# Optimization experiments

Hardware: AMD Instinct MI355X
Metric: run time of the kernel (lower is better)

The kernel has to match this reference:

```python
import jax, jax.numpy as jnp
import numpy as np

EPS = 1e-5
K = 20  # knn3(K=20) is hardcoded in the torch module


def _bn_lrelu(x, g, b, axes):
    # training-mode BatchNorm (batch statistics) + LeakyReLU(0.2)
    m = jnp.mean(x, axis=axes, keepdims=True)
    v = jnp.var(x, axis=axes, keepdims=True)
    y = (x - m) * jax.lax.rsqrt(v + EPS) * g + b
    return jax.nn.leaky_relu(y, 0.2)


def _pool(pts, feat, num_pool):
    # pts: [B,N,3] coords, feat: [B,N,C]. KNN of first num_pool points vs all
    # points, gather neighbor features, max over the K neighbors.
    sub = pts[:, :num_pool]                                   # [B,M,3]
    d2 = (jnp.sum(sub * sub, -1)[:, :, None]
          + jnp.sum(pts * pts, -1)[:, None, :]
          - 2.0 * jnp.einsum('bmd,bnd->bmn', sub, pts))       # [B,M,N]
    idx = jax.lax.top_k(-d2, K)[1]                            # [B,M,K]
    gathered = jax.vmap(lambda f, i: f[i])(feat, idx)         # [B,M,K,C]
    return sub, jnp.max(gathered, axis=2)                     # [B,M,C]


def setup_inputs() -> dict:
    key = jax.random.key(0)
    ks = jax.random.split(key, 16)
    f32 = jnp.float32
    def n(k, shape, s):
        return jax.random.normal(k, shape, dtype=f32) * s
    emb = 1024
    return {
        'x': jax.random.normal(ks[0], (16, 3, 4096), dtype=f32),
        'w1': n(ks[1], (64, 3), 0.5), 'g1': jnp.ones(64, f32), 'b1': jnp.zeros(64, f32),
        'w2': n(ks[2], (64, 64), 0.12), 'g2': jnp.ones(64, f32), 'b2': jnp.zeros(64, f32),
        'w3': n(ks[3], (128, 64), 0.12), 'g3': jnp.ones(128, f32), 'b3': jnp.zeros(128, f32),
        'w4': n(ks[4], (256, 128), 0.09), 'g4': jnp.ones(256, f32), 'b4': jnp.zeros(256, f32),
        'w5': n(ks[5], (emb, 512), 0.045), 'g5': jnp.ones(emb, f32), 'b5': jnp.zeros(emb, f32),
        'l1w': n(ks[6], (512, 2 * emb), 0.022), 'g6': jnp.ones(512, f32), 'b6': jnp.zeros(512, f32),
        'l2w': n(ks[7], (256, 512), 0.045), 'l2b': jnp.zeros(256, f32),
        'g7': jnp.ones(256, f32), 'b7': jnp.zeros(256, f32),
        'l3w': n(ks[8], (40, 256), 0.06), 'l3b': jnp.zeros(40, f32),
    }


def reference(x, w1, g1, b1, w2, g2, b2, w3, g3, b3, w4, g4, b4,
              w5, g5, b5, l1w, g6, b6, l2w, l2b, g7, b7, l3w, l3b):
    B, _, N = x.shape
    pts = jnp.transpose(x, (0, 2, 1))                 # [B,N,3]
    f = _bn_lrelu(pts @ w1.T, g1, b1, (0, 1))         # conv1 -> [B,N,64]
    p, f = _pool(pts, f, N // 4)
    _, x1 = _pool(p, f, N // 64)                      # [B,N/64,64]
    f = _bn_lrelu(f @ w2.T, g2, b2, (0, 1))           # conv2
    p, f = _pool(p, f, N // 16)
    _, x2 = _pool(p, f, N // 64)                      # [B,N/64,64]
    f = _bn_lrelu(f @ w3.T, g3, b3, (0, 1))           # conv3
    p, f = _pool(p, f, N // 32)
    _, x3 = _pool(p, f, N // 64)                      # [B,N/64,128]
    f = _bn_lrelu(f @ w4.T, g4, b4, (0, 1))           # conv4
    p, f = _pool(p, f, N // 64)                       # [B,N/64,256]
    h = jnp.concatenate([x1, x2, x3, f], axis=-1)     # [B,N/64,512]
    h = _bn_lrelu(h @ w5.T, g5, b5, (0, 1))           # conv5 -> [B,N/64,emb]
    h = jnp.concatenate([jnp.max(h, axis=1), jnp.mean(h, axis=1)], axis=-1)
    h = _bn_lrelu(h @ l1w.T, g6, b6, (0,))            # linear1 (no bias)
    h = _bn_lrelu(h @ l2w.T + l2b, g7, b7, (0,))      # linear2; dropout = eval identity
    return h @ l3w.T + l3b                            # [B,40]
```

## Files before the change

kernel.cpp:

```cpp
#include <hip/hip_runtime.h>

#define BN_EPS 1e-5f
#define KNN 20

static inline int ceildiv(int a, int b) { return (a + b - 1) / b; }

__device__ __forceinline__ unsigned long long shflxor64(unsigned long long v, int m, int w) {
    int lo = __shfl_xor((int)(unsigned)(v & 0xffffffffull), m, w);
    int hi = __shfl_xor((int)(unsigned)(v >> 32), m, w);
    return ((unsigned long long)(unsigned)hi << 32) | (unsigned)lo;
}

__global__ void moments3_kernel(const float* __restrict__ x, int N,
                                float* __restrict__ part ,
                                float4* __restrict__ pk ) {
    int b = blockIdx.x;
    int chunk = blockIdx.y;
    int t = threadIdx.x;
    int n0 = chunk * (N >> 2);
    int n1 = n0 + (N >> 2);
    const float* xb = x + (size_t)b * 3 * N;
    float m[9] = {0, 0, 0, 0, 0, 0, 0, 0, 0};
    for (int n = n0 + t; n < n1; n += 256) {
        float px = xb[n], py = xb[N + n], pz = xb[2 * N + n];
        float nr = px * px + py * py + pz * pz;
        pk[(size_t)b * N + n] = make_float4(px, py, pz, nr);
        m[0] += px; m[1] += py; m[2] += pz;
        m[3] += px * px; m[4] += py * py; m[5] += pz * pz;
        m[6] += px * py; m[7] += px * pz; m[8] += py * pz;
    }
#pragma unroll
    for (int o = 32; o; o >>= 1)
#pragma unroll
        for (int i = 0; i < 9; ++i) m[i] += __shfl_down(m[i], o);
    __shared__ float red[4][9];
    if ((t & 63) == 0)
#pragma unroll
        for (int i = 0; i < 9; ++i) red[t >> 6][i] = m[i];
    __syncthreads();
    if (t == 0) {
#pragma unroll
        for (int i = 0; i < 9; ++i)
            part[(b * 4 + chunk) * 9 + i] = red[0][i] + red[1][i] + red[2][i] + red[3][i];
    }
}

__global__ void knn_all_kernel(const float4* __restrict__ pk, int Nstride,
                               int* __restrict__ iA, int* __restrict__ iB,
                               int* __restrict__ iC, int* __restrict__ iD,
                               int* __restrict__ iE, int* __restrict__ iF) {
    int b = blockIdx.y;
    int bx = blockIdx.x;
    int M, N; int* out; int qbase;
    if (bx < 128)      { M = 1024; N = 4096; out = iA; qbase = bx * 8; }
    else if (bx < 136) { M = 64;   N = 1024; out = iB; qbase = (bx - 128) * 8; }
    else if (bx < 168) { M = 256;  N = 1024; out = iC; qbase = (bx - 136) * 8; }
    else if (bx < 176) { M = 64;   N = 256;  out = iD; qbase = (bx - 168) * 8; }
    else if (bx < 192) { M = 128;  N = 256;  out = iE; qbase = (bx - 176) * 8; }
    else               { M = 64;   N = 128;  out = iF; qbase = (bx - 192) * 8; }
    int wave = threadIdx.x >> 6;
    int lane = threadIdx.x & 63;
    int sl = lane & 31;
    int half = lane >> 5;
    int q = qbase + wave * 2 + half;
    const float4* pb = pk + (size_t)b * Nstride;
    float4 qp = pb[q];

    auto dist = [&](int j) -> float {
        float4 c = pb[j];
        return qp.w + c.w - 2.f * (qp.x * c.x + qp.y * c.y + qp.z * c.z);
    };

    int up_addr = ((sl == 0) ? lane : (lane - 1)) << 2;
    int wd_addr = (19 + (half << 5)) << 2;
    int segbyte = half << 7;

    unsigned long long lk;
    {
        float d2 = dist(sl);
        unsigned u = __float_as_uint(d2);
        unsigned ok = (u & 0x80000000u) ? ~u : (u | 0x80000000u);
        lk = ((unsigned long long)ok << 32) | (unsigned)sl;
    }
#pragma unroll
    for (int size = 2; size <= 32; size <<= 1) {
#pragma unroll
        for (int stride = size >> 1; stride >= 1; stride >>= 1) {
            unsigned long long p = shflxor64(lk, stride, 32);
            bool ascend = (sl & size) == 0;
            bool low = (sl & stride) == 0;
            bool keepMin = (ascend == low);
            bool pLess = p < lk;
            lk = (keepMin == pLess) ? p : lk;
        }
    }
    unsigned okey = (unsigned)(lk >> 32);
    unsigned du = (okey & 0x80000000u) ? (okey ^ 0x80000000u) : ~okey;
    float ld = __uint_as_float(du);
    int li = (int)(unsigned)(lk & 0xffffffffull);
    float wd = __uint_as_float(__builtin_amdgcn_ds_bpermute(wd_addr, (int)__float_as_uint(ld)));

    auto insert2 = [&](float dc, int jb, unsigned long long msk) {
        unsigned mlo = (unsigned)msk, mhi = (unsigned)(msk >> 32);
        while (mlo | mhi) {
            int slo = __ffs((int)mlo) - 1;
            int shi = __ffs((int)mhi) - 1;
            int srcl = half ? shi : slo;
            int addr = ((srcl & 31) << 2) + segbyte;
            float d = __uint_as_float(__builtin_amdgcn_ds_bpermute(addr, (int)__float_as_uint(dc)));
            if (srcl < 0) d = 3.4e38f;
            int id = jb + (srcl & 31);
            float up_d = __uint_as_float(__builtin_amdgcn_ds_bpermute(up_addr, (int)__float_as_uint(ld)));
            int up_i = __builtin_amdgcn_ds_bpermute(up_addr, li);
            bool c = d < ld;
            bool cp = (sl != 0) && (d < up_d);
            ld = c ? (cp ? up_d : d) : ld;
            li = c ? (cp ? up_i : id) : li;
            mlo &= mlo - 1;
            mhi &= mhi - 1;
        }
    };

    {
        float dc = dist(32 + sl);
        unsigned long long m = __ballot(dc < wd);
        if (m) {
            insert2(dc, 32, m);
            wd = __uint_as_float(__builtin_amdgcn_ds_bpermute(wd_addr, (int)__float_as_uint(ld)));
        }
    }
    for (int j0 = 64; j0 < N; j0 += 64) {
        float dc0 = dist(j0 + sl);
        float dc1 = dist(j0 + 32 + sl);
        unsigned long long m0 = __ballot(dc0 < wd);
        unsigned long long m1 = __ballot(dc1 < wd);
        if (m0 | m1) {
            if (m0) insert2(dc0, j0, m0);
            if (m1) insert2(dc1, j0 + 32, m1);
            wd = __uint_as_float(__builtin_amdgcn_ds_bpermute(wd_addr, (int)__float_as_uint(ld)));
        }
    }
    if (sl < KNN) out[((size_t)b * M + q) * KNN + sl] = li;
}

__global__ void pool1_kernel(const float4* __restrict__ pk, int N, const int* __restrict__ idxA,
                             const float* __restrict__ w1, const float* __restrict__ mom,
                             const float* __restrict__ g, const float* __restrict__ bb,
                             float Rinv, int nparts, float* __restrict__ out, int M) {
    __shared__ float S[9];
    __shared__ float sca[64], shb[64];
    int c = threadIdx.x;
    int tid = threadIdx.y * 64 + c;
    if (tid < 9) {
        float s = 0.f;
        for (int bi = 0; bi < nparts; ++bi) s += mom[bi * 9 + tid];
        S[tid] = s;
    }
    __syncthreads();
    if (tid < 64) {
        float wx = w1[tid * 3], wy = w1[tid * 3 + 1], wz = w1[tid * 3 + 2];
        float mean = (wx * S[0] + wy * S[1] + wz * S[2]) * Rinv;
        float e2 = (wx * wx * S[3] + wy * wy * S[4] + wz * wz * S[5] +
                    2.f * (wx * wy * S[6] + wx * wz * S[7] + wy * wz * S[8])) * Rinv;
        float var = e2 - mean * mean;
        float a = g[tid] * rsqrtf(var + BN_EPS);
        sca[tid] = a;
        shb[tid] = bb[tid] - mean * a;
    }
    __syncthreads();
    int m = blockIdx.x * 4 + threadIdx.y;
    int b = blockIdx.y;
    const float4* pb = pk + (size_t)b * N;
    const int* ip = idxA + ((size_t)b * M + m) * KNN;
    float wx = w1[c * 3], wy = w1[c * 3 + 1], wz = w1[c * 3 + 2];
    float mx = -3.4e38f, mn = 3.4e38f;
#pragma unroll
    for (int k = 0; k < KNN; ++k) {
        float4 p = pb[ip[k]];
        float d = wx * p.x + wy * p.y + wz * p.z;
        mx = fmaxf(mx, d); mn = fminf(mn, d);
    }
    float a = sca[c];
    float v = a * (a >= 0.f ? mx : mn) + shb[c];
    out[((size_t)b * M + m) * 64 + c] = v >= 0.f ? v : 0.2f * v;
}

__global__ void pool_bn_kernel(const float* __restrict__ f, const int* __restrict__ idx,
                               float* __restrict__ out, int M, int Nf, int C,
                               int out_stride, int out_off, const float* __restrict__ scsh) {
    int c = threadIdx.x;
    int m = blockIdx.x * blockDim.y + threadIdx.y;
    int b = blockIdx.y;
    const int* ip = idx + ((size_t)b * M + m) * KNN;
    const float* fb = f + (size_t)b * Nf * C;
    float mx = -3.4e38f, mn = 3.4e38f;
#pragma unroll
    for (int k = 0; k < KNN; ++k) {
        int j = ip[k];
        float v = fb[(size_t)j * C + c];
        mx = fmaxf(mx, v);
        mn = fminf(mn, v);
    }
    float a = scsh[c];
    float v = a * (a >= 0.f ? mx : mn) + scsh[C + c];
    v = v >= 0.f ? v : 0.2f * v;
    out[((size_t)b * M + m) * out_stride + out_off + c] = v;
}

template <int BM, bool POOL>
__global__ void gemm_kernel(const float* __restrict__ A, const float* __restrict__ W,
                            float* __restrict__ Cout, int M, int N, int K,
                            float* __restrict__ part , int nbn,
                            const float* __restrict__ pf, const int* __restrict__ pidx,
                            float* __restrict__ pout, int pNf, int pC, int pstride, int poff) {
    constexpr int RM = BM / 16;
    int t = threadIdx.x;
    int nbm = M / BM;
    int bx = blockIdx.x;
    if (POOL && bx >= nbm * nbn) {
        int e = bx - nbm * nbn;
        int rows = 256 / pC;
        int bpb = 64 / rows;
        int b = e / bpb, mi = e % bpb;
        int m = mi * rows + t / pC;
        int c = t % pC;
        const int* ip = pidx + ((size_t)b * 64 + m) * KNN;
        const float* fb = pf + (size_t)b * pNf * pC;
        float mx = -3.4e38f;
#pragma unroll
        for (int k = 0; k < KNN; ++k) mx = fmaxf(mx, fb[(size_t)ip[k] * pC + c]);
        pout[((size_t)b * 64 + m) * pstride + poff + c] = mx;
        return;
    }
    int bm = bx / nbn, bn = bx % nbn;
    __shared__ float As[16][BM + 4], Ws[16][68];
    int tx = t & 15, ty = t >> 4;
    const float* Ab = A + (size_t)bm * BM * K;
    const float* Wb = W + (size_t)bn * 64 * K;
    float acc[RM][4] = {};
    int srow = t >> 2, skb = (t & 3) << 2;
    for (int k0 = 0; k0 < K; k0 += 16) {
        if (t < BM * 4) {
            float4 av = *(const float4*)&Ab[(size_t)srow * K + k0 + skb];
            As[skb][srow] = av.x; As[skb + 1][srow] = av.y;
            As[skb + 2][srow] = av.z; As[skb + 3][srow] = av.w;
        }
        {
            float4 wv = *(const float4*)&Wb[(size_t)srow * K + k0 + skb];
            Ws[skb][srow] = wv.x; Ws[skb + 1][srow] = wv.y;
            Ws[skb + 2][srow] = wv.z; Ws[skb + 3][srow] = wv.w;
        }
        __syncthreads();
#pragma unroll
        for (int kk = 0; kk < 16; ++kk) {
            float av[RM];
#pragma unroll
            for (int i = 0; i < RM; ++i) av[i] = As[kk][ty * RM + i];
            float4 w4 = *(const float4*)&Ws[kk][tx * 4];
            float wv[4] = {w4.x, w4.y, w4.z, w4.w};
#pragma unroll
            for (int i = 0; i < RM; ++i)
#pragma unroll
                for (int j = 0; j < 4; ++j) acc[i][j] += av[i] * wv[j];
        }
        __syncthreads();
    }
#pragma unroll
    for (int i = 0; i < RM; ++i) {
        float4 v = make_float4(acc[i][0], acc[i][1], acc[i][2], acc[i][3]);
        *(float4*)&Cout[(size_t)(bm * BM + ty * RM + i) * N + bn * 64 + tx * 4] = v;
    }
    __shared__ float2 sred[16][64];
#pragma unroll
    for (int j = 0; j < 4; ++j) {
        float s = 0.f, q = 0.f;
#pragma unroll
        for (int i = 0; i < RM; ++i) { s += acc[i][j]; q += acc[i][j] * acc[i][j]; }
        sred[ty][tx * 4 + j] = make_float2(s, q);
    }
    __syncthreads();
    if (t < 64) {
        float s = 0.f, q = 0.f;
#pragma unroll
        for (int r = 0; r < 16; ++r) { s += sred[r][t].x; q += sred[r][t].y; }
        part[(size_t)bm * 2 * N + bn * 64 + t] = s;
        part[(size_t)bm * 2 * N + N + bn * 64 + t] = q;
    }
}

__global__ void bn_finalize_kernel(const float* __restrict__ part, int nparts, int C, int R,
                                   const float* __restrict__ g, const float* __restrict__ bb,
                                   float* __restrict__ scsh) {
    int c = blockIdx.x;
    int t = threadIdx.x;
    float s = 0.f, q = 0.f;
    for (int k = t; k < nparts; k += 256) {
        s += part[(size_t)k * 2 * C + c];
        q += part[(size_t)k * 2 * C + C + c];
    }
#pragma unroll
    for (int o = 32; o; o >>= 1) { s += __shfl_down(s, o); q += __shfl_down(q, o); }
    __shared__ float2 red[4];
    if ((t & 63) == 0) red[t >> 6] = make_float2(s, q);
    __syncthreads();
    if (t == 0) {
        s = red[0].x + red[1].x + red[2].x + red[3].x;
        q = red[0].y + red[1].y + red[2].y + red[3].y;
        float mean = s / (float)R;
        float var = q / (float)R - mean * mean;
        float a = g[c] * rsqrtf(var + BN_EPS);
        scsh[c] = a;
        scsh[C + c] = bb[c] - mean * a;
    }
}

__global__ void global_pool_bn_kernel(const float* __restrict__ h,
                                      const float* __restrict__ scsh,
                                      float* __restrict__ out) {
    int c = blockIdx.x * 256 + threadIdx.x;
    int b = blockIdx.y;
    const float* hb = h + (size_t)b * 64 * 1024;
    float a = scsh[c], sh = scsh[1024 + c];
    float mx = -3.4e38f, s = 0.f;
    for (int r = 0; r < 64; ++r) {
        float v = a * hb[r * 1024 + c] + sh;
        v = v >= 0.f ? v : 0.2f * v;
        mx = fmaxf(mx, v); s += v;
    }
    out[b * 2048 + c] = mx;
    out[b * 2048 + 1024 + c] = s * (1.f / 64.f);
}

__global__ void head_gemm_wide(const float* __restrict__ A, const float* __restrict__ W,
                               float* __restrict__ out, int N, int K) {
    __shared__ float red[4][64];
    int t = threadIdx.x;
    int m = blockIdx.y;
    int nl = t & 63, kq = t >> 6;
    int n = blockIdx.x * 64 + nl;
    int Kc = K >> 2;
    const float4* a4 = (const float4*)(A + (size_t)m * K + kq * Kc);
    const float4* w4 = (const float4*)(W + (size_t)n * K + kq * Kc);
    float s = 0.f;
    for (int k = 0; k < (Kc >> 2); ++k) {
        float4 a = a4[k], w = w4[k];
        s += a.x * w.x + a.y * w.y + a.z * w.z + a.w * w.w;
    }
    red[kq][nl] = s;
    __syncthreads();
    if (t < 64)
        out[(size_t)m * N + blockIdx.x * 64 + t] = red[0][t] + red[1][t] + red[2][t] + red[3][t];
}

__global__ void head_bn_gemm2(const float* __restrict__ Apre,
                              const float* __restrict__ g, const float* __restrict__ bb,
                              const float* __restrict__ W, const float* __restrict__ bias,
                              float* __restrict__ out) {
    __shared__ float An[512];
    __shared__ float red[4][64];
    int t = threadIdx.x;
    int m = blockIdx.y;
    for (int c = t; c < 512; c += 256) {
        float s = 0.f, q = 0.f, vm = 0.f;
#pragma unroll
        for (int r = 0; r < 16; ++r) {
            float v = Apre[r * 512 + c];
            s += v; q += v * v;
            if (r == m) vm = v;
        }
        float mean = s * (1.f / 16.f);
        float var = q * (1.f / 16.f) - mean * mean;
        float a = g[c] * rsqrtf(var + BN_EPS);
        float v = a * (vm - mean) + bb[c];
        An[c] = v >= 0.f ? v : 0.2f * v;
    }
    __syncthreads();
    int nl = t & 63, kq = t >> 6;
    int n = blockIdx.x * 64 + nl;
    const float* wn = W + (size_t)n * 512 + kq * 128;
    const float* an = An + kq * 128;
    float s = 0.f;
    for (int k = 0; k < 128; k += 4) {
        float4 a4 = *(const float4*)&an[k];
        float4 w4 = *(const float4*)&wn[k];
        s += a4.x * w4.x + a4.y * w4.y + a4.z * w4.z + a4.w * w4.w;
    }
    red[kq][nl] = s;
    __syncthreads();
    if (t < 64) {
        float r = red[0][t] + red[1][t] + red[2][t] + red[3][t];
        out[(size_t)m * 256 + blockIdx.x * 64 + t] = r + bias[blockIdx.x * 64 + t];
    }
}

__global__ void head_bn_gemm3(const float* __restrict__ Apre,
                              const float* __restrict__ g, const float* __restrict__ bb,
                              const float* __restrict__ W, const float* __restrict__ bias,
                              float* __restrict__ out) {
    __shared__ float An[256];
    __shared__ float red[4][64];
    int t = threadIdx.x;
    int m = blockIdx.x;
    {
        int c = t;
        float s = 0.f, q = 0.f, vm = 0.f;
#pragma unroll
        for (int r = 0; r < 16; ++r) {
            float v = Apre[r * 256 + c];
            s += v; q += v * v;
            if (r == m) vm = v;
        }
        float mean = s * (1.f / 16.f);
        float var = q * (1.f / 16.f) - mean * mean;
        float a = g[c] * rsqrtf(var + BN_EPS);
        float v = a * (vm - mean) + bb[c];
        An[c] = v >= 0.f ? v : 0.2f * v;
    }
    __syncthreads();
    int nl = t & 63, kq = t >> 6;
    float s = 0.f;
    if (nl < 40) {
        const float* wn = W + (size_t)nl * 256 + kq * 64;
        const float* an = An + kq * 64;
        for (int k = 0; k < 64; k += 4) {
            float4 a4 = *(const float4*)&an[k];
            float4 w4 = *(const float4*)&wn[k];
            s += a4.x * w4.x + a4.y * w4.y + a4.z * w4.z + a4.w * w4.w;
        }
    }
    red[kq][nl] = s;
    __syncthreads();
    if (t < 40) {
        float r = red[0][t] + red[1][t] + red[2][t] + red[3][t];
        out[(size_t)m * 40 + t] = r + bias[t];
    }
}

extern "C" void kernel_launch(void* const* d_in, const int* in_sizes, int n_in,
                              void* d_out, int out_size, void* d_ws, size_t ws_size,
                              hipStream_t stream) {
    const int B = 16, N = 4096;
    const float* x   = (const float*)d_in[0];
    const float* w1  = (const float*)d_in[1];
    const float* g1  = (const float*)d_in[2];
    const float* b1  = (const float*)d_in[3];
    const float* w2  = (const float*)d_in[4];
    const float* g2  = (const float*)d_in[5];
    const float* b2  = (const float*)d_in[6];
    const float* w3  = (const float*)d_in[7];
    const float* g3  = (const float*)d_in[8];
    const float* b3  = (const float*)d_in[9];
    const float* w4  = (const float*)d_in[10];
    const float* g4  = (const float*)d_in[11];
    const float* b4  = (const float*)d_in[12];
    const float* w5  = (const float*)d_in[13];
    const float* g5  = (const float*)d_in[14];
    const float* b5  = (const float*)d_in[15];
    const float* l1w = (const float*)d_in[16];
    const float* g6  = (const float*)d_in[17];
    const float* b6  = (const float*)d_in[18];
    const float* l2w = (const float*)d_in[19];
    const float* l2b = (const float*)d_in[20];
    const float* g7  = (const float*)d_in[21];
    const float* b7  = (const float*)d_in[22];
    const float* l3w = (const float*)d_in[23];
    const float* l3b = (const float*)d_in[24];
    float* outp = (float*)d_out;

    char* ws = (char*)d_ws;
    size_t off = 0;
    auto alloc = [&](size_t bytes) -> void* {
        void* p = ws + off;
        off += (bytes + 255) & ~(size_t)255;
        return p;
    };
    float* f1p   = (float*)alloc((size_t)B * 1024 * 64 * 4);
    float* f2pre = (float*)alloc((size_t)B * 1024 * 64 * 4);
    float* f2p   = (float*)alloc((size_t)B * 256 * 64 * 4);
    float* f3pre = (float*)alloc((size_t)B * 256 * 128 * 4);
    float* f3p   = (float*)alloc((size_t)B * 128 * 128 * 4);
    float* f4pre = (float*)alloc((size_t)B * 128 * 256 * 4);
    float* hcat  = (float*)alloc((size_t)B * 64 * 512 * 4);
    float* h5pre = (float*)alloc((size_t)B * 64 * 1024 * 4);
    float* hg    = (float*)alloc((size_t)B * 2048 * 4);
    float* h6pre = (float*)alloc((size_t)B * 512 * 4);
    float* h7pre = (float*)alloc((size_t)B * 256 * 4);
    int* idxA = (int*)alloc((size_t)B * 1024 * KNN * 4);
    int* idxB = (int*)alloc((size_t)B * 64 * KNN * 4);
    int* idxC = (int*)alloc((size_t)B * 256 * KNN * 4);
    int* idxD = (int*)alloc((size_t)B * 64 * KNN * 4);
    int* idxE = (int*)alloc((size_t)B * 128 * KNN * 4);
    int* idxF = (int*)alloc((size_t)B * 64 * KNN * 4);
    float* mom   = (float*)alloc((size_t)B * 4 * 9 * 4);
    float4* pkbuf = (float4*)alloc((size_t)B * N * 16);
    float* part2 = (float*)alloc((size_t)512 * 2 * 64 * 4);
    float* part3 = (float*)alloc((size_t)128 * 2 * 128 * 4);
    float* part4 = (float*)alloc((size_t)64 * 2 * 256 * 4);
    float* part5 = (float*)alloc((size_t)32 * 2 * 1024 * 4);
    float* sc2 = (float*)alloc(2 * 64 * 4);
    float* sc3 = (float*)alloc(2 * 128 * 4);
    float* sc4 = (float*)alloc(2 * 256 * 4);
    float* sc5 = (float*)alloc(2 * 1024 * 4);

    moments3_kernel<<<dim3(B, 4), 256, 0, stream>>>(x, N, mom, pkbuf);
    knn_all_kernel<<<dim3(200, B), 256, 0, stream>>>(pkbuf, N, idxA, idxB, idxC, idxD, idxE, idxF);

    pool1_kernel<<<dim3(256, B), dim3(64, 4), 0, stream>>>(pkbuf, N, idxA, w1, mom, g1, b1,
                                                           1.f / (B * N), B * 4, f1p, 1024);

    gemm_kernel<32, true><<<dim3(512 + 256), 256, 0, stream>>>(
        f1p, w2, f2pre, B * 1024, 64, 64, part2, 1,
        f1p, idxB, hcat, 1024, 64, 512, 0);
    bn_finalize_kernel<<<dim3(64), 256, 0, stream>>>(part2, 512, 64, B * 1024, g2, b2, sc2);
    pool_bn_kernel<<<dim3(64, B), dim3(64, 4), 0, stream>>>(f2pre, idxC, f2p, 256, 1024, 64, 64, 0, sc2);

    gemm_kernel<32, true><<<dim3(256 + 256), 256, 0, stream>>>(
        f2p, w3, f3pre, B * 256, 128, 64, part3, 2,
        f2p, idxD, hcat, 256, 64, 512, 64);
    bn_finalize_kernel<<<dim3(128), 256, 0, stream>>>(part3, 128, 128, B * 256, g3, b3, sc3);
    pool_bn_kernel<<<dim3(64, B), dim3(128, 2), 0, stream>>>(f3pre, idxE, f3p, 128, 256, 128, 128, 0, sc3);

    gemm_kernel<32, true><<<dim3(256 + 512), 256, 0, stream>>>(
        f3p, w4, f4pre, B * 128, 256, 128, part4, 4,
        f3p, idxF, hcat, 128, 128, 512, 128);
    bn_finalize_kernel<<<dim3(256), 256, 0, stream>>>(part4, 64, 256, B * 128, g4, b4, sc4);
    pool_bn_kernel<<<dim3(64, B), dim3(256, 1), 0, stream>>>(f4pre, idxF, hcat, 64, 128, 256, 512, 256, sc4);

    gemm_kernel<32, false><<<dim3(512), 256, 0, stream>>>(
        hcat, w5, h5pre, B * 64, 1024, 512, part5, 16,
        nullptr, nullptr, nullptr, 0, 1, 0, 0);
    bn_finalize_kernel<<<dim3(1024), 256, 0, stream>>>(part5, 32, 1024, B * 64, g5, b5, sc5);
    global_pool_bn_kernel<<<dim3(4, B), 256, 0, stream>>>(h5pre, sc5, hg);

    head_gemm_wide<<<dim3(8, B), 256, 0, stream>>>(hg, l1w, h6pre, 512, 2048);
    head_bn_gemm2<<<dim3(4, B), 256, 0, stream>>>(h6pre, g6, b6, l2w, l2b, h7pre);
    head_bn_gemm3<<<dim3(B), 256, 0, stream>>>(h7pre, g7, b7, l3w, l3b, outp);
}
```

Measured before the change: 246.9 us.

## Fuse BN finalize into GEMMs via last-block atomics and unroll KNN scan

Removes the separate bn_finalize launches by having the last-finishing GEMM block, found with an atomic counter and threadfence, reduce the partial sums and write scale/shift. It also folds head_bn_gemm3 into head_bn_gemm2 the same way. Separately, the KNN scan loop now handles 128 candidates per step so the threshold refresh and branch run less often. This cuts several kernel launches, but the final reduction now runs serially in a single block, and the counters need a memset on every call.

Measured after the change: 410.2 us. 1.66x slower.

```diff
diff --git a/kernel.cpp b/kernel.cpp
--- a/kernel.cpp
+++ b/kernel.cpp
@@ -129,16 +129,31 @@
             wd = __uint_as_float(__builtin_amdgcn_ds_bpermute(wd_addr, (int)__float_as_uint(ld)));
         }
     }
-    for (int j0 = 64; j0 < N; j0 += 64) {
+    int j0 = 64;
+    for (; j0 + 128 <= N; j0 += 128) {
+        float dc0 = dist(j0 + sl);
+        float dc1 = dist(j0 + 32 + sl);
+        float dc2 = dist(j0 + 64 + sl);
+        float dc3 = dist(j0 + 96 + sl);
+        unsigned long long m0 = __ballot(dc0 < wd);
+        unsigned long long m1 = __ballot(dc1 < wd);
+        unsigned long long m2 = __ballot(dc2 < wd);
+        unsigned long long m3 = __ballot(dc3 < wd);
+        if (m0 | m1 | m2 | m3) {
+            if (m0) insert2(dc0, j0, m0);
+            if (m1) insert2(dc1, j0 + 32, m1);
+            if (m2) insert2(dc2, j0 + 64, m2);
+            if (m3) insert2(dc3, j0 + 96, m3);
+            wd = __uint_as_float(__builtin_amdgcn_ds_bpermute(wd_addr, (int)__float_as_uint(ld)));
+        }
+    }
+    if (j0 < N) {
         float dc0 = dist(j0 + sl);
         float dc1 = dist(j0 + 32 + sl);
         unsigned long long m0 = __ballot(dc0 < wd);
         unsigned long long m1 = __ballot(dc1 < wd);
-        if (m0 | m1) {
-            if (m0) insert2(dc0, j0, m0);
-            if (m1) insert2(dc1, j0 + 32, m1);
-            wd = __uint_as_float(__builtin_amdgcn_ds_bpermute(wd_addr, (int)__float_as_uint(ld)));
-        }
+        if (m0) insert2(dc0, j0, m0);
+        if (m1) insert2(dc1, j0 + 32, m1);
     }
     if (sl < KNN) out[((size_t)b * M + q) * KNN + sl] = li;
 }
@@ -211,6 +226,8 @@
 __global__ void gemm_kernel(const float* __restrict__ A, const float* __restrict__ W,
                             float* __restrict__ Cout, int M, int N, int K,
                             float* __restrict__ part , int nbn,
+                            int* __restrict__ cnt, float* __restrict__ scsh,
+                            const float* __restrict__ g, const float* __restrict__ bb, int R,
                             const float* __restrict__ pf, const int* __restrict__ pidx,
                             float* __restrict__ pout, int pNf, int pC, int pstride, int poff) {
     constexpr int RM = BM / 16;
@@ -234,6 +251,8 @@
     }
     int bm = bx / nbn, bn = bx % nbn;
     __shared__ float As[16][BM + 4], Ws[16][68];
+    __shared__ float2 sred[16][64];
+    __shared__ int lastflag;
     int tx = t & 15, ty = t >> 4;
     const float* Ab = A + (size_t)bm * BM * K;
     const float* Wb = W + (size_t)bn * 64 * K;
@@ -270,7 +289,6 @@
         float4 v = make_float4(acc[i][0], acc[i][1], acc[i][2], acc[i][3]);
         *(float4*)&Cout[(size_t)(bm * BM + ty * RM + i) * N + bn * 64 + tx * 4] = v;
     }
-    __shared__ float2 sred[16][64];
 #pragma unroll
     for (int j = 0; j < 4; ++j) {
         float s = 0.f, q = 0.f;
@@ -286,31 +304,35 @@
         part[(size_t)bm * 2 * N + bn * 64 + t] = s;
         part[(size_t)bm * 2 * N + N + bn * 64 + t] = q;
     }
-}
-
-__global__ void bn_finalize_kernel(const float* __restrict__ part, int nparts, int C, int R,
-                                   const float* __restrict__ g, const float* __restrict__ bb,
-                                   float* __restrict__ scsh) {
-    int c = blockIdx.x;
-    int t = threadIdx.x;
-    float s = 0.f, q = 0.f;
-    for (int k = t; k < nparts; k += 256) {
-        s += part[(size_t)k * 2 * C + c];
-        q += part[(size_t)k * 2 * C + C + c];
-    }
-#pragma unroll
-    for (int o = 32; o; o >>= 1) { s += __shfl_down(s, o); q += __shfl_down(q, o); }
-    __shared__ float2 red[4];
-    if ((t & 63) == 0) red[t >> 6] = make_float2(s, q);
     __syncthreads();
     if (t == 0) {
-        s = red[0].x + red[1].x + red[2].x + red[3].x;
-        q = red[0].y + red[1].y + red[2].y + red[3].y;
-        float mean = s / (float)R;
-        float var = q / (float)R - mean * mean;
-        float a = g[c] * rsqrtf(var + BN_EPS);
-        scsh[c] = a;
-        scsh[C + c] = bb[c] - mean * a;
+        __threadfence();
+        int old = atomicAdd(cnt, 1);
+        lastflag = (old == nbm * nbn - 1);
+    }
+    __syncthreads();
+    if (!lastflag) return;
+    __threadfence();
+    for (int c0 = 0; c0 < N; c0 += 64) {
+        int c = c0 + (t & 63);
+        int pc = t >> 6;
+        float s = 0.f, q = 0.f;
+        for (int k = pc; k < nbm; k += 4) {
+            s += part[(size_t)k * 2 * N + c];
+            q += part[(size_t)k * 2 * N + N + c];
+        }
+        sred[pc][t & 63] = make_float2(s, q);
+        __syncthreads();
+        if (t < 64) {
+            float ss = sred[0][t].x + sred[1][t].x + sred[2][t].x + sred[3][t].x;
+            float qq = sred[0][t].y + sred[1][t].y + sred[2][t].y + sred[3][t].y;
+            float mean = ss / (float)R;
+            float var = qq / (float)R - mean * mean;
+            float a = g[c0 + t] * rsqrtf(var + BN_EPS);
+            scsh[c0 + t] = a;
+            scsh[N + c0 + t] = bb[c0 + t] - mean * a;
+        }
+        __syncthreads();
     }
 }
 
@@ -355,9 +377,14 @@
 __global__ void head_bn_gemm2(const float* __restrict__ Apre,
                               const float* __restrict__ g, const float* __restrict__ bb,
                               const float* __restrict__ W, const float* __restrict__ bias,
-                              float* __restrict__ out) {
+                              float* __restrict__ out7, int* __restrict__ cnt,
+                              const float* __restrict__ g7, const float* __restrict__ bb7,
+                              const float* __restrict__ W3, const float* __restrict__ bias3,
+                              float* __restrict__ outp) {
     __shared__ float An[512];
     __shared__ float red[4][64];
+    __shared__ float An3[16][257];
+    __shared__ int lastflag;
     int t = threadIdx.x;
     int m = blockIdx.y;
     for (int c = t; c < 512; c += 256) {
@@ -389,50 +416,46 @@
     __syncthreads();
     if (t < 64) {
         float r = red[0][t] + red[1][t] + red[2][t] + red[3][t];
-        out[(size_t)m * 256 + blockIdx.x * 64 + t] = r + bias[blockIdx.x * 64 + t];
-    }
-}
-
-__global__ void head_bn_gemm3(const float* __restrict__ Apre,
-                              const float* __restrict__ g, const float* __restrict__ bb,
-                              const float* __restrict__ W, const float* __restrict__ bias,
-                              float* __restrict__ out) {
-    __shared__ float An[256];
-    __shared__ float red[4][64];
-    int t = threadIdx.x;
-    int m = blockIdx.x;
+        out7[(size_t)m * 256 + blockIdx.x * 64 + t] = r + bias[blockIdx.x * 64 + t];
+    }
+    __syncthreads();
+    if (t == 0) {
+        __threadfence();
+        int old = atomicAdd(cnt, 1);
+        lastflag = (old == 4 * 16 - 1);
+    }
+    __syncthreads();
+    if (!lastflag) return;
+    __threadfence();
     {
         int c = t;
-        float s = 0.f, q = 0.f, vm = 0.f;
+        float vals[16];
+        float ss = 0.f, qq = 0.f;
 #pragma unroll
         for (int r = 0; r < 16; ++r) {
-            float v = Apre[r * 256 + c];
-            s += v; q += v * v;
-            if (r == m) vm = v;
-        }
-        float mean = s * (1.f / 16.f);
-        float var = q * (1.f / 16.f) - mean * mean;
-        float a = g[c] * rsqrtf(var + BN_EPS);
-        float v = a * (vm - mean) + bb[c];
-        An[c] = v >= 0.f ? v : 0.2f * v;
-    }
-    __syncthreads();
-    int nl = t & 63, kq = t >> 6;
-    float s = 0.f;
-    if (nl < 40) {
-        const float* wn = W + (size_t)nl * 256 + kq * 64;
-        const float* an = An + kq * 64;
-        for (int k = 0; k < 64; k += 4) {
-            float4 a4 = *(const float4*)&an[k];
-            float4 w4 = *(const float4*)&wn[k];
-            s += a4.x * w4.x + a4.y * w4.y + a4.z * w4.z + a4.w * w4.w;
-        }
-    }
-    red[kq][nl] = s;
-    __syncthreads();
-    if (t < 40) {
-        float r = red[0][t] + red[1][t] + red[2][t] + red[3][t];
-        out[(size_t)m * 40 + t] = r + bias[t];
+            float v = out7[r * 256 + c];
+            vals[r] = v; ss += v; qq += v * v;
+        }
+        float mean = ss * (1.f / 16.f);
+        float var = qq * (1.f / 16.f) - mean * mean;
+        float a = g7[c] * rsqrtf(var + BN_EPS);
+        float sh = bb7[c] - mean * a;
+#pragma unroll
+        for (int r = 0; r < 16; ++r) {
+            float v = a * vals[r] + sh;
+            An3[r][c] = v >= 0.f ? v : 0.2f * v;
+        }
+    }
+    __syncthreads();
+    for (int o = t; o < 16 * 40; o += 256) {
+        int mm = o / 40, nn = o % 40;
+        const float* w3 = W3 + (size_t)nn * 256;
+        float acc = 0.f;
+        for (int k = 0; k < 256; k += 4) {
+            acc += An3[mm][k] * w3[k] + An3[mm][k + 1] * w3[k + 1] +
+                   An3[mm][k + 2] * w3[k + 2] + An3[mm][k + 3] * w3[k + 3];
+        }
+        outp[(size_t)mm * 40 + nn] = acc + bias3[nn];
     }
 }
 
@@ -501,6 +524,9 @@
     float* sc3 = (float*)alloc(2 * 128 * 4);
     float* sc4 = (float*)alloc(2 * 256 * 4);
     float* sc5 = (float*)alloc(2 * 1024 * 4);
+    int* cnts  = (int*)alloc(8 * 4);
+
+    hipMemsetAsync(cnts, 0, 8 * 4, stream);
 
     moments3_kernel<<<dim3(B, 4), 256, 0, stream>>>(x, N, mom, pkbuf);
     knn_all_kernel<<<dim3(200, B), 256, 0, stream>>>(pkbuf, N, idxA, idxB, idxC, idxD, idxE, idxF);
@@ -510,29 +536,29 @@
 
     gemm_kernel<32, true><<<dim3(512 + 256), 256, 0, stream>>>(
         f1p, w2, f2pre, B * 1024, 64, 64, part2, 1,
+        cnts + 0, sc2, g2, b2, B * 1024,
         f1p, idxB, hcat, 1024, 64, 512, 0);
-    bn_finalize_kernel<<<dim3(64), 256, 0, stream>>>(part2, 512, 64, B * 1024, g2, b2, sc2);
     pool_bn_kernel<<<dim3(64, B), dim3(64, 4), 0, stream>>>(f2pre, idxC, f2p, 256, 1024, 64, 64, 0, sc2);
 
     gemm_kernel<32, true><<<dim3(256 + 256), 256, 0, stream>>>(
         f2p, w3, f3pre, B * 256, 128, 64, part3, 2,
+        cnts + 1, sc3, g3, b3, B * 256,
         f2p, idxD, hcat, 256, 64, 512, 64);
-    bn_finalize_kernel<<<dim3(128), 256, 0, stream>>>(part3, 128, 128, B * 256, g3, b3, sc3);
     pool_bn_kernel<<<dim3(64, B), dim3(128, 2), 0, stream>>>(f3pre, idxE, f3p, 128, 256, 128, 128, 0, sc3);
 
     gemm_kernel<32, true><<<dim3(256 + 512), 256, 0, stream>>>(
         f3p, w4, f4pre, B * 128, 256, 128, part4, 4,
+        cnts + 2, sc4, g4, b4, B * 128,
         f3p, idxF, hcat, 128, 128, 512, 128);
-    bn_finalize_kernel<<<dim3(256), 256, 0, stream>>>(part4, 64, 256, B * 128, g4, b4, sc4);
     pool_bn_kernel<<<dim3(64, B), dim3(256, 1), 0, stream>>>(f4pre, idxF, hcat, 64, 128, 256, 512, 256, sc4);
 
     gemm_kernel<32, false><<<dim3(512), 256, 0, stream>>>(
         hcat, w5, h5pre, B * 64, 1024, 512, part5, 16,
+        cnts + 3, sc5, g5, b5, B * 64,
         nullptr, nullptr, nullptr, 0, 1, 0, 0);
-    bn_finalize_kernel<<<dim3(1024), 256, 0, stream>>>(part5, 32, 1024, B * 64, g5, b5, sc5);
     global_pool_bn_kernel<<<dim3(4, B), 256, 0, stream>>>(h5pre, sc5, hg);
 
     head_gemm_wide<<<dim3(8, B), 256, 0, stream>>>(hg, l1w, h6pre, 512, 2048);
-    head_bn_gemm2<<<dim3(4, B), 256, 0, stream>>>(h6pre, g6, b6, l2w, l2b, h7pre);
-    head_bn_gemm3<<<dim3(B), 256, 0, stream>>>(h7pre, g7, b7, l3w, l3b, outp);
-}
+    head_bn_gemm2<<<dim3(4, B), 256, 0, stream>>>(h6pre, g6, b6, l2w, l2b, h7pre,
+                                                  cnts + 4, g7, b7, l3w, l3b, outp);
+}
```
